# Kernel optimization log

Hardware: AMD Instinct MI355X
Metric: run time of the kernel (lower is better)

The kernel has to match this reference:

```python
import jax, jax.numpy as jnp
import numpy as np

N_NODES = 100000
N_EDGES = 3200000
N_FEAT = 512
HIDDEN = 16
N_CLASS = 7


def gcn_conv(x, edge_index, W, b, n_nodes):
    """PyG GCNConv (add_self_loops=True, symmetric normalization).
    x: [N, F_in]; edge_index: [2, E] with row=source, col=target.
    """
    h = x @ W  # [N, F_out] -- linear transform before aggregation (F_out small)
    src, dst = edge_index[0], edge_index[1]
    # degree computed on target column (incl. self-loop), as in PyG gcn_norm
    deg = jax.ops.segment_sum(jnp.ones(src.shape[0], dtype=h.dtype), dst,
                              num_segments=n_nodes) + 1.0
    dinv = jax.lax.rsqrt(deg)  # deg >= 1 always (self-loops)
    norm = dinv[src] * dinv[dst]  # [E]
    msg = norm[:, None] * h[src]  # [E, F_out]
    agg = jax.ops.segment_sum(msg, dst, num_segments=n_nodes)
    # self-loop contribution: norm_ii = dinv_i^2
    agg = agg + (dinv * dinv)[:, None] * h
    return agg + b


def setup_inputs() -> dict:
    key = jax.random.key(0)
    k1, k2, k3, k4 = jax.random.split(key, 4)
    x = jax.random.normal(k1, (N_NODES, N_FEAT), dtype=jnp.float32)
    edge_index = jax.random.randint(k2, (2, N_EDGES), 0, N_NODES, dtype=jnp.int64)
    W1 = jax.random.normal(k3, (N_FEAT, HIDDEN), dtype=jnp.float32) * (1.0 / np.sqrt(N_FEAT))
    b1 = jnp.zeros((HIDDEN,), dtype=jnp.float32)
    W2 = jax.random.normal(k4, (HIDDEN, N_CLASS), dtype=jnp.float32) * (1.0 / np.sqrt(HIDDEN))
    b2 = jnp.zeros((N_CLASS,), dtype=jnp.float32)
    return {"x": x, "edge_index": edge_index, "W1": W1, "b1": b1, "W2": W2, "b2": b2}


def reference(x, edge_index, W1, b1, W2, b2):
    n = x.shape[0]
    h = gcn_conv(x, edge_index, W1, b1, n)
    h = jax.nn.relu(h)
    # F.dropout in eval mode is identity (deterministic reference)
    h = gcn_conv(h, edge_index, W2, b2, n)
    return jax.nn.log_softmax(h, axis=1)
```

## Files before the change

### kernel.cpp

```cpp
#include <hip/hip_runtime.h>
#include <math.h>


#define F_IN 512
#define HID  16
#define NCLS 7
#define NCHUNK 256
#define BK 64
#define NBMAX 1600
#define CAP 3072
#define WT_STRIDE 516

static __device__ __forceinline__ float bf2f(unsigned short u) {
    union { unsigned int i; float f; } v; v.i = ((unsigned int)u) << 16; return v.f;
}
static __device__ __forceinline__ unsigned short f2bf(float f) {
    union { float f; unsigned int u; } v; v.f = f;
    unsigned int b = v.u;
    return (unsigned short)((b + 0x7FFFu + ((b >> 16) & 1u)) >> 16);
}

__global__ __launch_bounds__(256) void k_a1(const int* __restrict__ ei, int E, int perChunk,
                                            int nb, int* __restrict__ bh) {
    __shared__ int hist[NBMAX];
    for (int t = threadIdx.x; t < nb; t += 256) hist[t] = 0;
    __syncthreads();
    const int* dst = ei + E;
    int c = blockIdx.x;
    int s0 = c * perChunk;
    int s1 = min(s0 + perChunk, E);
    for (int e = s0 + threadIdx.x; e < s1; e += 256)
        atomicAdd(&hist[dst[e] >> 6], 1);
    __syncthreads();
    for (int t = threadIdx.x; t < nb; t += 256) bh[(size_t)c * nb + t] = hist[t];
}

__global__ __launch_bounds__(256) void k_a2a(int* __restrict__ bh, int nb,
                                             int* __restrict__ Tb) {
    __shared__ int sd[256];
    int b = blockIdx.x, tid = threadIdx.x;
    int v = bh[(size_t)tid * nb + b];
    sd[tid] = v;
    __syncthreads();
    for (int off = 1; off < 256; off <<= 1) {
        int t = (tid >= off) ? sd[tid - off] : 0;
        __syncthreads();
        sd[tid] += t;
        __syncthreads();
    }
    bh[(size_t)tid * nb + b] = sd[tid] - v;
    if (tid == 255) Tb[b] = sd[255];
}

__global__ __launch_bounds__(256) void k_a2b(const int* __restrict__ Tb, int nb,
                                             int* __restrict__ Bb) {
    __shared__ int sd[256];
    int tid = threadIdx.x;
    int carry = 0;
    for (int base = 0; base < nb; base += 256) {
        int v = (base + tid < nb) ? Tb[base + tid] : 0;
        sd[tid] = v;
        __syncthreads();
        for (int off = 1; off < 256; off <<= 1) {
            int t = (tid >= off) ? sd[tid - off] : 0;
            __syncthreads();
            sd[tid] += t;
            __syncthreads();
        }
        if (base + tid < nb) Bb[base + tid] = carry + sd[tid] - v;
        carry += sd[255];
        __syncthreads();
    }
}

__global__ __launch_bounds__(256) void k_a3(const int* __restrict__ ei, int E, int perChunk,
                                            int nb, const int* __restrict__ bh,
                                            const int* __restrict__ Bb,
                                            unsigned* __restrict__ part) {
    __shared__ int cur[NBMAX];
    __shared__ int baseL[NBMAX];
    int c = blockIdx.x;
    for (int t = threadIdx.x; t < nb; t += 256) {
        cur[t] = 0;
        baseL[t] = Bb[t] + bh[(size_t)c * nb + t];
    }
    __syncthreads();
    const int* src = ei;
    const int* dst = ei + E;
    int s0 = c * perChunk;
    int s1 = min(s0 + perChunk, E);
    for (int e = s0 + threadIdx.x; e < s1; e += 256) {
        int s = src[e], d = dst[e];
        int b = d >> 6;
        int r = atomicAdd(&cur[b], 1);
        part[baseL[b] + r] = ((unsigned)(d & (BK - 1)) << 20) | (unsigned)s;
    }
}

__global__ __launch_bounds__(256) void k_b(const unsigned* __restrict__ part,
                                           const int* __restrict__ Tb,
                                           const int* __restrict__ Bb,
                                           int* __restrict__ csr, int* __restrict__ cnt,
                                           int* __restrict__ offs, float* __restrict__ dinv,
                                           int N) {
    __shared__ unsigned eL[CAP];
    __shared__ int hist[BK], sd[BK], cur[BK];
    int b = blockIdx.x, tid = threadIdx.x;
    int base = Bb[b], ct = Tb[b];
    if (tid < BK) hist[tid] = 0;
    __syncthreads();
    for (int k = tid; k < ct; k += 256) {
        unsigned v = part[base + k];
        if (k < CAP) eL[k] = v;
        atomicAdd(&hist[v >> 20], 1);
    }
    __syncthreads();
    if (tid < BK) sd[tid] = hist[tid];
    __syncthreads();
    for (int off = 1; off < BK; off <<= 1) {
        int t = 0;
        if (tid < BK && tid >= off) t = sd[tid - off];
        __syncthreads();
        if (tid < BK) sd[tid] += t;
        __syncthreads();
    }
    if (tid < BK) {
        int h = hist[tid];
        int ex = sd[tid] - h;
        cur[tid] = ex;
        int node = b * BK + tid;
        if (node < N) {
            cnt[node] = h;
            offs[node] = base + ex;
            dinv[node] = rsqrtf((float)h + 1.0f);
        }
    }
    __syncthreads();
    for (int k = tid; k < ct; k += 256) {
        unsigned v = (k < CAP) ? eL[k] : part[base + k];
        int dl = (int)(v >> 20);
        int r = atomicAdd(&cur[dl], 1);
        csr[base + r] = (int)(v & 0xFFFFFu);
    }
}

__global__ __launch_bounds__(256) void k_gemm1(const float* __restrict__ x,
                                               const float* __restrict__ W1,
                                               const float* __restrict__ dinv,
                                               unsigned short* __restrict__ hs1b,
                                               int N) {
    __shared__ float wlT[HID * WT_STRIDE];
    {
        int j = threadIdx.x & 15;
        int k0 = threadIdx.x >> 4;
        for (int it = 0; it < F_IN / 16; ++it) {
            int k = k0 + 16 * it;
            wlT[j * WT_STRIDE + k] = W1[k * HID + j];
        }
    }
    __syncthreads();

    int lane = threadIdx.x & 15;
    int g = threadIdx.x >> 4;
    int rbase = blockIdx.x * 64 + g * 4;

    const float* xp0 = x + (size_t)(rbase + 0 < N ? rbase + 0 : 0) * F_IN + 4 * lane;
    const float* xp1 = x + (size_t)(rbase + 1 < N ? rbase + 1 : 0) * F_IN + 4 * lane;
    const float* xp2 = x + (size_t)(rbase + 2 < N ? rbase + 2 : 0) * F_IN + 4 * lane;
    const float* xp3 = x + (size_t)(rbase + 3 < N ? rbase + 3 : 0) * F_IN + 4 * lane;

    float acc[4][16];
#pragma unroll
    for (int r = 0; r < 4; ++r)
#pragma unroll
        for (int j = 0; j < 16; ++j) acc[r][j] = 0.0f;

#pragma unroll 2
    for (int p = 0; p < 8; ++p) {
        float4 a0 = *(const float4*)(xp0 + 64 * p);
        float4 a1 = *(const float4*)(xp1 + 64 * p);
        float4 a2 = *(const float4*)(xp2 + 64 * p);
        float4 a3 = *(const float4*)(xp3 + 64 * p);
        const float* wb = &wlT[64 * p + 4 * lane];
#pragma unroll
        for (int j = 0; j < 16; ++j) {
            float4 w4 = *(const float4*)(wb + (size_t)j * WT_STRIDE);
            acc[0][j] = fmaf(a0.x, w4.x, fmaf(a0.y, w4.y, fmaf(a0.z, w4.z, fmaf(a0.w, w4.w, acc[0][j]))));
            acc[1][j] = fmaf(a1.x, w4.x, fmaf(a1.y, w4.y, fmaf(a1.z, w4.z, fmaf(a1.w, w4.w, acc[1][j]))));
            acc[2][j] = fmaf(a2.x, w4.x, fmaf(a2.y, w4.y, fmaf(a2.z, w4.z, fmaf(a2.w, w4.w, acc[2][j]))));
            acc[3][j] = fmaf(a3.x, w4.x, fmaf(a3.y, w4.y, fmaf(a3.z, w4.z, fmaf(a3.w, w4.w, acc[3][j]))));
        }
    }

    bool b8 = (lane & 8) != 0, b4 = (lane & 4) != 0, b2 = (lane & 2) != 0, b1 = (lane & 1) != 0;
#pragma unroll
    for (int r = 0; r < 4; ++r) {
#pragma unroll
        for (int j = 0; j < 8; ++j) {
            float lo = acc[r][j], hi = acc[r][j + 8];
            float keep = b8 ? hi : lo;
            float send = b8 ? lo : hi;
            acc[r][j] = keep + __shfl_xor(send, 8, 16);
        }
#pragma unroll
        for (int j = 0; j < 4; ++j) {
            float lo = acc[r][j], hi = acc[r][j + 4];
            float keep = b4 ? hi : lo;
            float send = b4 ? lo : hi;
            acc[r][j] = keep + __shfl_xor(send, 4, 16);
        }
#pragma unroll
        for (int j = 0; j < 2; ++j) {
            float lo = acc[r][j], hi = acc[r][j + 2];
            float keep = b2 ? hi : lo;
            float send = b2 ? lo : hi;
            acc[r][j] = keep + __shfl_xor(send, 2, 16);
        }
        {
            float lo = acc[r][0], hi = acc[r][1];
            float keep = b1 ? hi : lo;
            float send = b1 ? lo : hi;
            acc[r][0] = keep + __shfl_xor(send, 1, 16);
        }
        int row = rbase + r;
        if (row < N)
            hs1b[(size_t)row * HID + lane] = f2bf(dinv[row] * acc[r][0]);
    }
}

__global__ __launch_bounds__(256) void k_agg1(const int* __restrict__ csr,
                                              const int* __restrict__ offs,
                                              const int* __restrict__ cnt,
                                              const float* __restrict__ dinv,
                                              const unsigned short* __restrict__ hs1b,
                                              const float* __restrict__ b1,
                                              const float* __restrict__ W2,
                                              float* __restrict__ hs2, int N) {
    int lane = threadIdx.x & 15;
    int i = blockIdx.x * 16 + (threadIdx.x >> 4);
    float w2r[NCLS];
#pragma unroll
    for (int c = 0; c < NCLS; c++) w2r[c] = W2[lane * NCLS + c];
    float b1l = b1[lane];
    if (i >= N) return;
    int start = offs[i], end = start + cnt[i];
    float acc = bf2f(hs1b[(size_t)i * HID + lane]);
    int k = start;
    for (; k + 3 < end; k += 4) {
        int s0 = csr[k], s1 = csr[k + 1], s2 = csr[k + 2], s3 = csr[k + 3];
        float v0 = bf2f(hs1b[(size_t)s0 * HID + lane]);
        float v1 = bf2f(hs1b[(size_t)s1 * HID + lane]);
        float v2 = bf2f(hs1b[(size_t)s2 * HID + lane]);
        float v3 = bf2f(hs1b[(size_t)s3 * HID + lane]);
        acc += (v0 + v1) + (v2 + v3);
    }
    for (; k < end; k++)
        acc += bf2f(hs1b[(size_t)csr[k] * HID + lane]);
    float v = fmaf(dinv[i], acc, b1l);
    float hr = v > 0.0f ? v : 0.0f;
    float dv = dinv[i];
    float res[NCLS];
#pragma unroll
    for (int c = 0; c < NCLS; c++) {
        float t = hr * w2r[c];
#pragma unroll
        for (int w = 8; w >= 1; w >>= 1) t += __shfl_xor(t, w, 16);
        res[c] = t;
    }
    if (lane < NCLS) {
        float o = res[0];
#pragma unroll
        for (int c = 1; c < NCLS; c++) o = (lane == c) ? res[c] : o;
        hs2[(size_t)i * NCLS + lane] = dv * o;
    }
}

__global__ __launch_bounds__(256) void k_agg2(const int* __restrict__ csr,
                                              const int* __restrict__ offs,
                                              const int* __restrict__ cnt,
                                              const float* __restrict__ dinv,
                                              const float* __restrict__ hs2,
                                              const float* __restrict__ b2,
                                              float* __restrict__ out, int N) {
    int lane = threadIdx.x & 7;
    int i = blockIdx.x * 32 + (threadIdx.x >> 3);
    if (i >= N) return;
    int cc = lane < NCLS ? lane : NCLS - 1;
    int start = offs[i], end = start + cnt[i];
    float acc = hs2[(size_t)i * NCLS + cc];
    int k = start;
    for (; k + 3 < end; k += 4) {
        int s0 = csr[k], s1 = csr[k + 1], s2 = csr[k + 2], s3 = csr[k + 3];
        float v0 = hs2[(size_t)s0 * NCLS + cc];
        float v1 = hs2[(size_t)s1 * NCLS + cc];
        float v2 = hs2[(size_t)s2 * NCLS + cc];
        float v3 = hs2[(size_t)s3 * NCLS + cc];
        acc += (v0 + v1) + (v2 + v3);
    }
    for (; k < end; k++)
        acc += hs2[(size_t)csr[k] * NCLS + cc];
    float v = fmaf(dinv[i], acc, b2[cc]);
    float vm = (lane < NCLS) ? v : -INFINITY;
    float m = vm;
#pragma unroll
    for (int w = 4; w >= 1; w >>= 1) m = fmaxf(m, __shfl_xor(m, w, 8));
    float e = (lane < NCLS) ? expf(v - m) : 0.0f;
    float ssum = e;
#pragma unroll
    for (int w = 4; w >= 1; w >>= 1) ssum += __shfl_xor(ssum, w, 8);
    if (lane < NCLS) out[(size_t)i * NCLS + lane] = v - m - logf(ssum);
}

extern "C" void kernel_launch(void* const* d_in, const int* in_sizes, int n_in,
                              void* d_out, int out_size, void* d_ws, size_t ws_size,
                              hipStream_t stream) {
    const float* x  = (const float*)d_in[0];
    const int*   ei = (const int*)d_in[1];
    const float* W1 = (const float*)d_in[2];
    const float* b1 = (const float*)d_in[3];
    const float* W2 = (const float*)d_in[4];
    const float* b2 = (const float*)d_in[5];
    float* out = (float*)d_out;

    const int N = in_sizes[0] / F_IN;
    const int E = in_sizes[1] / 2;
    const int nb = (N + BK - 1) / BK;
    const int perChunk = (E + NCHUNK - 1) / NCHUNK;

    unsigned* w = (unsigned*)d_ws;
    auto al4 = [](size_t v) { return (v + 3) & ~(size_t)3; };
    size_t o = 0;
    unsigned*       part = w + o;               o = al4(o + E);
    int*            csr  = (int*)(w + o);       o = al4(o + E);
    unsigned short* hs1b = (unsigned short*)(w + o); o = al4(o + (size_t)N * HID / 2);
    float*          hs2  = (float*)(w + o);     o = al4(o + (size_t)N * NCLS);
    float*          dinv = (float*)(w + o);     o = al4(o + N);
    int*            cnt  = (int*)(w + o);       o = al4(o + N);
    int*            offs = (int*)(w + o);       o = al4(o + (size_t)NCHUNK * nb > 0 ? o + N - N + N : N), o = al4(o);
    o = 0;
    part = w + o;                               o = al4(o + E);
    csr  = (int*)(w + o);                       o = al4(o + E);
    hs1b = (unsigned short*)(w + o);            o = al4(o + (size_t)N * HID / 2);
    hs2  = (float*)(w + o);                     o = al4(o + (size_t)N * NCLS);
    dinv = (float*)(w + o);                     o = al4(o + N);
    cnt  = (int*)(w + o);                       o = al4(o + N);
    offs = (int*)(w + o);                       o = al4(o + N);
    int*            bh   = (int*)(w + o);       o = al4(o + (size_t)NCHUNK * nb);
    int*            Tb   = (int*)(w + o);       o = al4(o + nb);
    int*            Bb   = (int*)(w + o);

    k_a1<<<NCHUNK, 256, 0, stream>>>(ei, E, perChunk, nb, bh);
    k_a2a<<<nb, 256, 0, stream>>>(bh, nb, Tb);
    k_a2b<<<1, 256, 0, stream>>>(Tb, nb, Bb);
    k_a3<<<NCHUNK, 256, 0, stream>>>(ei, E, perChunk, nb, bh, Bb, part);
    k_b<<<nb, 256, 0, stream>>>(part, Tb, Bb, csr, cnt, offs, dinv, N);
    k_gemm1<<<(N + 63) / 64, 256, 0, stream>>>(x, W1, dinv, hs1b, N);
    k_agg1<<<(N + 15) / 16, 256, 0, stream>>>(csr, offs, cnt, dinv, hs1b, b1, W2, hs2, N);
    k_agg2<<<(N + 31) / 32, 256, 0, stream>>>(csr, offs, cnt, dinv, hs2, b2, out, N);
}
```

Before: 486.7 us.

## Pack bf16 pairs per lane, cooperative CSR index loads, pad hs2 rows to 8

The first aggregation now uses 8 lanes per node, each loading a packed pair of bf16 features as one 32-bit word, so each group handles two features per lane and the grid covers 32 nodes per block. Both aggregation kernels load 8 CSR neighbour indices cooperatively and broadcast them with shuffles, replacing redundant per-lane index loads. The second layer's intermediate is padded to 8 floats per row, stored in the reused partition buffer, for aligned 32-byte gathers. This cuts index traffic and load instruction count, in exchange for more shuffles and a padded intermediate.

```diff
diff --git a/kernel.cpp b/kernel.cpp
--- a/kernel.cpp
+++ b/kernel.cpp
@@ -232,73 +232,94 @@
                                               const int* __restrict__ offs,
                                               const int* __restrict__ cnt,
                                               const float* __restrict__ dinv,
-                                              const unsigned short* __restrict__ hs1b,
+                                              const unsigned* __restrict__ hs1u,
                                               const float* __restrict__ b1,
                                               const float* __restrict__ W2,
-                                              float* __restrict__ hs2, int N) {
-    int lane = threadIdx.x & 15;
-    int i = blockIdx.x * 16 + (threadIdx.x >> 4);
-    float w2r[NCLS];
-#pragma unroll
-    for (int c = 0; c < NCLS; c++) w2r[c] = W2[lane * NCLS + c];
-    float b1l = b1[lane];
+                                              float* __restrict__ hs2p, int N) {
+    int lane = threadIdx.x & 7;
+    int i = blockIdx.x * 32 + (threadIdx.x >> 3);
+    float w2a[NCLS], w2b[NCLS];
+#pragma unroll
+    for (int c = 0; c < NCLS; c++) {
+        w2a[c] = W2[(2 * lane) * NCLS + c];
+        w2b[c] = W2[(2 * lane + 1) * NCLS + c];
+    }
+    float b1a = b1[2 * lane], b1b = b1[2 * lane + 1];
     if (i >= N) return;
-    int start = offs[i], end = start + cnt[i];
-    float acc = bf2f(hs1b[(size_t)i * HID + lane]);
-    int k = start;
-    for (; k + 3 < end; k += 4) {
-        int s0 = csr[k], s1 = csr[k + 1], s2 = csr[k + 2], s3 = csr[k + 3];
-        float v0 = bf2f(hs1b[(size_t)s0 * HID + lane]);
-        float v1 = bf2f(hs1b[(size_t)s1 * HID + lane]);
-        float v2 = bf2f(hs1b[(size_t)s2 * HID + lane]);
-        float v3 = bf2f(hs1b[(size_t)s3 * HID + lane]);
-        acc += (v0 + v1) + (v2 + v3);
-    }
-    for (; k < end; k++)
-        acc += bf2f(hs1b[(size_t)csr[k] * HID + lane]);
-    float v = fmaf(dinv[i], acc, b1l);
-    float hr = v > 0.0f ? v : 0.0f;
+    int start = offs[i], cn = cnt[i];
+    unsigned su = hs1u[(size_t)i * 8 + lane];
+    float accA = __uint_as_float(su << 16);
+    float accB = __uint_as_float(su & 0xffff0000u);
+    int full = cn & ~7;
+    for (int k = 0; k < full; k += 8) {
+        int ev = csr[start + k + lane];
+#pragma unroll
+        for (int t = 0; t < 8; ++t) {
+            int s = __shfl(ev, t, 8);
+            unsigned u = hs1u[(size_t)s * 8 + lane];
+            accA += __uint_as_float(u << 16);
+            accB += __uint_as_float(u & 0xffff0000u);
+        }
+    }
+    int rem = cn - full;
+    if (rem) {
+        int ev = (lane < rem) ? csr[start + full + lane] : 0;
+        for (int t = 0; t < rem; ++t) {
+            int s = __shfl(ev, t, 8);
+            unsigned u = hs1u[(size_t)s * 8 + lane];
+            accA += __uint_as_float(u << 16);
+            accB += __uint_as_float(u & 0xffff0000u);
+        }
+    }
     float dv = dinv[i];
+    float vA = fmaf(dv, accA, b1a);
+    float vB = fmaf(dv, accB, b1b);
+    float hA = vA > 0.0f ? vA : 0.0f;
+    float hB = vB > 0.0f ? vB : 0.0f;
     float res[NCLS];
 #pragma unroll
     for (int c = 0; c < NCLS; c++) {
-        float t = hr * w2r[c];
-#pragma unroll
-        for (int w = 8; w >= 1; w >>= 1) t += __shfl_xor(t, w, 16);
+        float t = fmaf(hA, w2a[c], hB * w2b[c]);
+#pragma unroll
+        for (int w = 4; w >= 1; w >>= 1) t += __shfl_xor(t, w, 8);
         res[c] = t;
     }
-    if (lane < NCLS) {
-        float o = res[0];
-#pragma unroll
-        for (int c = 1; c < NCLS; c++) o = (lane == c) ? res[c] : o;
-        hs2[(size_t)i * NCLS + lane] = dv * o;
-    }
+    float o = res[0];
+#pragma unroll
+    for (int c = 1; c < NCLS; c++) o = (lane == c) ? res[c] : o;
+    hs2p[(size_t)i * 8 + lane] = dv * o;
 }
 
 __global__ __launch_bounds__(256) void k_agg2(const int* __restrict__ csr,
                                               const int* __restrict__ offs,
                                               const int* __restrict__ cnt,
                                               const float* __restrict__ dinv,
-                                              const float* __restrict__ hs2,
+                                              const float* __restrict__ hs2p,
                                               const float* __restrict__ b2,
                                               float* __restrict__ out, int N) {
     int lane = threadIdx.x & 7;
     int i = blockIdx.x * 32 + (threadIdx.x >> 3);
     if (i >= N) return;
+    int start = offs[i], cn = cnt[i];
+    float acc = hs2p[(size_t)i * 8 + lane];
+    int full = cn & ~7;
+    for (int k = 0; k < full; k += 8) {
+        int ev = csr[start + k + lane];
+#pragma unroll
+        for (int t = 0; t < 8; ++t) {
+            int s = __shfl(ev, t, 8);
+            acc += hs2p[(size_t)s * 8 + lane];
+        }
+    }
+    int rem = cn - full;
+    if (rem) {
+        int ev = (lane < rem) ? csr[start + full + lane] : 0;
+        for (int t = 0; t < rem; ++t) {
+            int s = __shfl(ev, t, 8);
+            acc += hs2p[(size_t)s * 8 + lane];
+        }
+    }
     int cc = lane < NCLS ? lane : NCLS - 1;
-    int start = offs[i], end = start + cnt[i];
-    float acc = hs2[(size_t)i * NCLS + cc];
-    int k = start;
-    for (; k + 3 < end; k += 4) {
-        int s0 = csr[k], s1 = csr[k + 1], s2 = csr[k + 2], s3 = csr[k + 3];
-        float v0 = hs2[(size_t)s0 * NCLS + cc];
-        float v1 = hs2[(size_t)s1 * NCLS + cc];
-        float v2 = hs2[(size_t)s2 * NCLS + cc];
-        float v3 = hs2[(size_t)s3 * NCLS + cc];
-        acc += (v0 + v1) + (v2 + v3);
-    }
-    for (; k < end; k++)
-        acc += hs2[(size_t)csr[k] * NCLS + cc];
     float v = fmaf(dinv[i], acc, b2[cc]);
     float vm = (lane < NCLS) ? v : -INFINITY;
     float m = vm;
@@ -330,21 +351,13 @@
     unsigned* w = (unsigned*)d_ws;
     auto al4 = [](size_t v) { return (v + 3) & ~(size_t)3; };
     size_t o = 0;
-    unsigned*       part = w + o;               o = al4(o + E);
+    unsigned*       part = w + o;
+    float*          hs2p = (float*)(w + o);     o = al4(o + E);
     int*            csr  = (int*)(w + o);       o = al4(o + E);
     unsigned short* hs1b = (unsigned short*)(w + o); o = al4(o + (size_t)N * HID / 2);
-    float*          hs2  = (float*)(w + o);     o = al4(o + (size_t)N * NCLS);
     float*          dinv = (float*)(w + o);     o = al4(o + N);
     int*            cnt  = (int*)(w + o);       o = al4(o + N);
-    int*            offs = (int*)(w + o);       o = al4(o + (size_t)NCHUNK * nb > 0 ? o + N - N + N : N), o = al4(o);
-    o = 0;
-    part = w + o;                               o = al4(o + E);
-    csr  = (int*)(w + o);                       o = al4(o + E);
-    hs1b = (unsigned short*)(w + o);            o = al4(o + (size_t)N * HID / 2);
-    hs2  = (float*)(w + o);                     o = al4(o + (size_t)N * NCLS);
-    dinv = (float*)(w + o);                     o = al4(o + N);
-    cnt  = (int*)(w + o);                       o = al4(o + N);
-    offs = (int*)(w + o);                       o = al4(o + N);
+    int*            offs = (int*)(w + o);       o = al4(o + N);
     int*            bh   = (int*)(w + o);       o = al4(o + (size_t)NCHUNK * nb);
     int*            Tb   = (int*)(w + o);       o = al4(o + nb);
     int*            Bb   = (int*)(w + o);
@@ -355,6 +368,7 @@
     k_a3<<<NCHUNK, 256, 0, stream>>>(ei, E, perChunk, nb, bh, Bb, part);
     k_b<<<nb, 256, 0, stream>>>(part, Tb, Bb, csr, cnt, offs, dinv, N);
     k_gemm1<<<(N + 63) / 64, 256, 0, stream>>>(x, W1, dinv, hs1b, N);
-    k_agg1<<<(N + 15) / 16, 256, 0, stream>>>(csr, offs, cnt, dinv, hs1b, b1, W2, hs2, N);
-    k_agg2<<<(N + 31) / 32, 256, 0, stream>>>(csr, offs, cnt, dinv, hs2, b2, out, N);
-}
+    k_agg1<<<(N + 31) / 32, 256, 0, stream>>>(csr, offs, cnt, dinv,
+                                              (const unsigned*)hs1b, b1, W2, hs2p, N);
+    k_agg2<<<(N + 31) / 32, 256, 0, stream>>>(csr, offs, cnt, dinv, hs2p, b2, out, N);
+}
```

Measured after the change: 477.7 us. Within noise of the previous version (-1.8%).
